# Kernel optimization log

Hardware: AMD Instinct MI355X
Metric: run time of the kernel (lower is better)

## Reference

```python
import jax, jax.numpy as jnp
import numpy as np

B, A, G = 256, 64, 978          # batch, n_atoms, num_gene
D_DRUG, D_CELL, D_DOSE = 128, 50, 128
CELL_IN, DOSE_IN = 978, 12
GLOBAL = D_DRUG + D_CELL + D_DOSE   # 306
EXP_IN = GLOBAL + 128               # 434
E, TOP_K = 4, 2


def setup_inputs() -> dict:
    key = jax.random.key(0)
    ks = jax.random.split(key, 24)
    w = lambda k, s: jax.random.normal(k, s, jnp.float32) * 0.05
    return {
        "drug_atom_embed": jax.random.normal(ks[0], (B, A, D_DRUG), jnp.float32),
        "input_cell_gex": jax.random.normal(ks[1], (B, CELL_IN), jnp.float32),
        "input_pert_idose": jax.random.normal(ks[2], (B, DOSE_IN), jnp.float32),
        # LinearEncoder: 978 -> 200 -> 100 -> 50 (ReLU after each)
        "cell_W1": w(ks[3], (CELL_IN, 200)), "cell_b1": jnp.zeros((200,), jnp.float32),
        "cell_W2": w(ks[4], (200, 100)),     "cell_b2": jnp.zeros((100,), jnp.float32),
        "cell_W3": w(ks[5], (100, D_CELL)),  "cell_b3": jnp.zeros((D_CELL,), jnp.float32),
        # DoseEncoder: 12 -> 64 -> 128 (ReLU after each; dropout off at eval)
        "dose_W1": w(ks[6], (DOSE_IN, 64)),  "dose_b1": jnp.zeros((64,), jnp.float32),
        "dose_W2": w(ks[7], (64, D_DOSE)),   "dose_b2": jnp.zeros((D_DOSE,), jnp.float32),
        # gene index embedding [num_gene, 128]
        "gene_emb": w(ks[8], (G, 128)),
        # GatingNetwork: 306 -> 128 -> 4
        "gate_W1": w(ks[9], (GLOBAL, 128)),  "gate_b1": jnp.zeros((128,), jnp.float32),
        "gate_W2": w(ks[10], (128, E)),      "gate_b2": jnp.zeros((E,), jnp.float32),
        # 4 ExpertNetworks stacked: 434 -> 128 -> 1
        "exp_W1": w(ks[11], (E, EXP_IN, 128)), "exp_b1": jnp.zeros((E, 128), jnp.float32),
        "exp_W2": w(ks[12], (E, 128, 1)),      "exp_b2": jnp.zeros((E, 1), jnp.float32),
    }


def reference(drug_atom_embed, input_cell_gex, input_pert_idose,
              cell_W1, cell_b1, cell_W2, cell_b2, cell_W3, cell_b3,
              dose_W1, dose_b1, dose_W2, dose_b2, gene_emb,
              gate_W1, gate_b1, gate_W2, gate_b2,
              exp_W1, exp_b1, exp_W2, exp_b2):
    relu = jax.nn.relu
    # drug: sum atom embeddings -> [B, 128]
    drug = drug_atom_embed.sum(axis=1)
    # cell encoder -> [B, 50]
    cell = relu(input_cell_gex @ cell_W1 + cell_b1)
    cell = relu(cell @ cell_W2 + cell_b2)
    cell = relu(cell @ cell_W3 + cell_b3)
    # dose encoder -> [B, 128]
    dose = relu(input_pert_idose @ dose_W1 + dose_b1)
    dose = relu(dose @ dose_W2 + dose_b2)
    # global features [B, 306]
    g = jnp.concatenate([drug, cell, dose], axis=1)
    # gating: top-k sparse gates [B, E]
    logits = relu(g @ gate_W1 + gate_b1) @ gate_W2 + gate_b2
    top_v, top_i = jax.lax.top_k(logits, TOP_K)
    top_g = jax.nn.softmax(top_v, axis=1)
    gates = jnp.zeros_like(logits).at[jnp.arange(logits.shape[0])[:, None], top_i].set(top_g)
    # gene-aware expert input [B, G, 434]
    expert_input = jnp.concatenate([
        jnp.broadcast_to(g[:, None, :], (g.shape[0], G, GLOBAL)),
        jnp.broadcast_to(gene_emb[None, :, :], (g.shape[0], G, 128)),
    ], axis=2)
    # all experts: [B, E, G, 128] -> [B, E, G]
    h = relu(jnp.einsum('bgi,eih->begh', expert_input, exp_W1) + exp_b1[None, :, None, :])
    o = jnp.einsum('begh,eho->beg', h, exp_W2) + exp_b2[None, :, :1]  # exp_b2[e,0] broadcast
    predictions = jnp.einsum('beg,be->bg', o, gates)
    return predictions, cell
```

## Files before the change

### kernel.cpp

```cpp
#include <hip/hip_runtime.h>

#define NB 256
#define NA 64
#define NG 978
#define CELL_IN 978
#define DOSE_IN 12
#define GLOBAL_F 306
#define EXP_IN 434
#define NE 4

#define WS_SEL 0
#define WS_U   (WS_SEL + NB*4)
#define WS_V   (WS_U + NB*256)

#define A_BLOCKS 256
#define AB_GRID  (NB + A_BLOCKS)

__device__ __forceinline__ float wave_reduce(float p) {
    #pragma unroll
    for (int off = 32; off > 0; off >>= 1) p += __shfl_down(p, off, 64);
    return p;
}

__global__ __launch_bounds__(1024) void ab_kernel(
    const float* __restrict__ drug, const float* __restrict__ gex,
    const float* __restrict__ idose,
    const float* __restrict__ cW1, const float* __restrict__ cb1,
    const float* __restrict__ cW2, const float* __restrict__ cb2,
    const float* __restrict__ cW3, const float* __restrict__ cb3,
    const float* __restrict__ dW1, const float* __restrict__ db1,
    const float* __restrict__ dW2, const float* __restrict__ db2,
    const float* __restrict__ gW1, const float* __restrict__ gb1,
    const float* __restrict__ gW2, const float* __restrict__ gb2,
    const float* __restrict__ eW1, const float* __restrict__ eb1,
    const float* __restrict__ gene,
    float* __restrict__ ws, float* __restrict__ cell_out)
{
    __shared__ float s_gex[CELL_IN];
    __shared__ float s_g[GLOBAL_F];
    __shared__ float s_h1[200];
    __shared__ float s_h2[100];
    __shared__ float s_gh[128];
    __shared__ float s_d1[64];
    __shared__ int   s_isel[2];
    __shared__ float s_part[16 * 200];
    __shared__ float s_pu[32 * 128];
    __shared__ float s_gene[64 * 129];

    const int blk = blockIdx.x, tid = threadIdx.x;

    if (blk >= NB) {
        const int ablk = blk - NB;
        const int tile = ablk >> 4, e = (ablk >> 2) & 3, hq = ablk & 3;

        for (int i = tid; i < 64 * 128; i += 1024) {
            int gl = i >> 7, k = i & 127;
            int g = tile * 64 + gl;
            s_gene[gl * 129 + k] = (g < NG) ? gene[g * 128 + k] : 0.f;
        }
        __syncthreads();

        const int slice = tid >> 6, g_in = tid & 63;
        const int h0 = hq * 32 + slice * 2;
        const float* wbase = eW1 + ((size_t)e * EXP_IN + GLOBAL_F) * 128 + h0;
        float a0 = 0.f, a1 = 0.f;
        #pragma unroll 8
        for (int k = 0; k < 128; ++k) {
            float x = s_gene[g_in * 129 + k];
            float2 w = *(const float2*)(wbase + (size_t)k * 128);
            a0 += x * w.x; a1 += x * w.y;
        }
        float* vout = ws + WS_V + ((size_t)tile * 512 + e * 128 + h0) * 64 + g_in;
        vout[0]  = a0;
        vout[64] = a1;
        return;
    }

    const int b = blk;

    if (tid < CELL_IN) s_gex[tid] = gex[b * CELL_IN + tid];
    {
        int row = tid >> 7, d = tid & 127;
        const float* p = drug + ((size_t)b * NA) * 128 + d;
        float acc = 0.f;
        #pragma unroll
        for (int i = 0; i < 8; ++i) acc += p[(size_t)(i * 8 + row) * 128];
        s_pu[row * 128 + d] = acc;
    }
    __syncthreads();
    if (tid < 128) {
        float a = 0.f;
        #pragma unroll
        for (int r = 0; r < 8; ++r) a += s_pu[r * 128 + tid];
        s_g[tid] = a;
    } else if (tid < 192) {
        int j = tid - 128;
        float acc = db1[j];
        #pragma unroll
        for (int i = 0; i < DOSE_IN; ++i)
            acc += idose[b * DOSE_IN + i] * dW1[i * 64 + j];
        s_d1[j] = fmaxf(acc, 0.f);
    }
    __syncthreads();
    if (tid < 128) {
        float acc = db2[tid];
        #pragma unroll 8
        for (int i = 0; i < 64; ++i) acc += s_d1[i] * dW2[i * 128 + tid];
        s_g[178 + tid] = fmaxf(acc, 0.f);
    }
    __syncthreads();

    {
        int q = tid & 63, ks = tid >> 6;
        if (q < 50) {
            int i0 = ks * 62, i1 = min(i0 + 62, CELL_IN);
            float4 acc = {0.f, 0.f, 0.f, 0.f};
            #pragma unroll 4
            for (int i = i0; i < i1; ++i) {
                float4 w = *(const float4*)(cW1 + (size_t)i * 200 + 4 * q);
                float x = s_gex[i];
                acc.x += x * w.x; acc.y += x * w.y; acc.z += x * w.z; acc.w += x * w.w;
            }
            *(float4*)(&s_part[ks * 200 + 4 * q]) = acc;
        }
    }
    __syncthreads();
    if (tid < 200) {
        float a = cb1[tid];
        #pragma unroll
        for (int ks = 0; ks < 16; ++ks) a += s_part[ks * 200 + tid];
        s_h1[tid] = fmaxf(a, 0.f);
    }
    __syncthreads();

    {
        int q = tid & 31, ks = tid >> 5;
        if (q < 25 && ks < 16) {
            int i0 = ks * 13, i1 = min(i0 + 13, 200);
            float4 acc = {0.f, 0.f, 0.f, 0.f};
            #pragma unroll
            for (int i = i0; i < i1; ++i) {
                float4 w = *(const float4*)(cW2 + (size_t)i * 100 + 4 * q);
                float x = s_h1[i];
                acc.x += x * w.x; acc.y += x * w.y; acc.z += x * w.z; acc.w += x * w.w;
            }
            *(float4*)(&s_part[ks * 100 + 4 * q]) = acc;
        }
    }
    __syncthreads();
    if (tid < 100) {
        float a = cb2[tid];
        #pragma unroll
        for (int ks = 0; ks < 16; ++ks) a += s_part[ks * 100 + tid];
        s_h2[tid] = fmaxf(a, 0.f);
    }
    __syncthreads();

    {
        int j = tid & 63, ks = tid >> 6;
        if (j < 50 && ks < 8) {
            int i0 = ks * 13, i1 = min(i0 + 13, 100);
            float acc = 0.f;
            #pragma unroll
            for (int i = i0; i < i1; ++i) acc += s_h2[i] * cW3[i * 50 + j];
            s_part[ks * 64 + j] = acc;
        }
    }
    __syncthreads();
    if (tid < 50) {
        float a = cb3[tid];
        #pragma unroll
        for (int ks = 0; ks < 8; ++ks) a += s_part[ks * 64 + tid];
        float r = fmaxf(a, 0.f);
        s_g[128 + tid] = r;
        cell_out[b * 50 + tid] = r;
    }
    __syncthreads();

    {
        int q = tid & 31, ks = tid >> 5;
        if (ks < 16) {
            int i0 = ks * 20, i1 = min(i0 + 20, GLOBAL_F);
            float4 acc = {0.f, 0.f, 0.f, 0.f};
            #pragma unroll
            for (int i = i0; i < i1; ++i) {
                float4 w = *(const float4*)(gW1 + (size_t)i * 128 + 4 * q);
                float x = s_g[i];
                acc.x += x * w.x; acc.y += x * w.y; acc.z += x * w.z; acc.w += x * w.w;
            }
            *(float4*)(&s_part[ks * 128 + 4 * q]) = acc;
        }
    }
    __syncthreads();
    if (tid < 128) {
        float a = gb1[tid];
        #pragma unroll
        for (int ks = 0; ks < 16; ++ks) a += s_part[ks * 128 + tid];
        s_gh[tid] = fmaxf(a, 0.f);
    }
    __syncthreads();

    if (tid < 64) {
        float h0 = s_gh[tid], h1 = s_gh[tid + 64];
        float logit[NE];
        #pragma unroll
        for (int j = 0; j < NE; ++j) {
            float p = h0 * gW2[tid * NE + j] + h1 * gW2[(tid + 64) * NE + j];
            p = wave_reduce(p);
            logit[j] = p + gb2[j];
        }
        if (tid == 0) {
            int i1 = 0; float v1 = logit[0];
            #pragma unroll
            for (int i = 1; i < NE; ++i) if (logit[i] > v1) { v1 = logit[i]; i1 = i; }
            int i2 = -1; float v2 = -__builtin_inff();
            #pragma unroll
            for (int i = 0; i < NE; ++i) {
                if (i == i1) continue;
                if (logit[i] > v2) { v2 = logit[i]; i2 = i; }
            }
            float ex = __expf(v2 - v1);
            float inv = 1.f / (1.f + ex);
            s_isel[0] = i1; s_isel[1] = i2;
            ws[WS_SEL + b * 4 + 0] = (float)i1;
            ws[WS_SEL + b * 4 + 1] = (float)i2;
            ws[WS_SEL + b * 4 + 2] = inv;
            ws[WS_SEL + b * 4 + 3] = ex * inv;
        }
    }
    __syncthreads();

    {
        int es = tid >> 9, ks = (tid >> 5) & 15, h4 = tid & 31;
        int e = s_isel[es];
        int i0 = ks * 20, i1 = min(i0 + 20, GLOBAL_F);
        const float* wp = eW1 + (size_t)e * EXP_IN * 128 + 4 * h4;
        float4 acc = {0.f, 0.f, 0.f, 0.f};
        #pragma unroll
        for (int i = i0; i < i1; ++i) {
            float4 w = *(const float4*)(wp + (size_t)i * 128);
            float x = s_g[i];
            acc.x += x * w.x; acc.y += x * w.y; acc.z += x * w.z; acc.w += x * w.w;
        }
        *(float4*)(&s_pu[(es * 16 + ks) * 128 + 4 * h4]) = acc;
    }
    __syncthreads();
    if (tid < 256) {
        int es = tid >> 7, h = tid & 127;
        int e = s_isel[es];
        float a = eb1[e * 128 + h];
        #pragma unroll
        for (int ks = 0; ks < 16; ++ks) a += s_pu[(es * 16 + ks) * 128 + h];
        ws[WS_U + (size_t)b * 256 + es * 128 + h] = a;
    }
}

__global__ __launch_bounds__(256) void c_kernel(
    const float* __restrict__ eW2, const float* __restrict__ eb2,
    const float* __restrict__ ws, float* __restrict__ pred)
{
    __shared__ float s_u[256];
    __shared__ float s_w2[256];
    const int b = blockIdx.x >> 2, quad = blockIdx.x & 3, tid = threadIdx.x;

    const int ea = (int)ws[WS_SEL + b * 4 + 0];
    const int eb = (int)ws[WS_SEL + b * 4 + 1];
    const float gA = ws[WS_SEL + b * 4 + 2];
    const float gB = ws[WS_SEL + b * 4 + 3];
    const float bA = eb2[ea], bB = eb2[eb];

    s_u[tid] = ws[WS_U + (size_t)b * 256 + tid];
    s_w2[tid] = (tid < 128) ? eW2[ea * 128 + tid] : eW2[eb * 128 + (tid - 128)];
    __syncthreads();

    const int wv = tid >> 6, lane = tid & 63;
    const int tile = quad * 4 + wv;
    const float* vA = ws + WS_V + ((size_t)tile * 512 + ea * 128) * 64 + lane;
    const float* vB = ws + WS_V + ((size_t)tile * 512 + eb * 128) * 64 + lane;

    float dA = 0.f, dB = 0.f;
    #pragma unroll 8
    for (int h = 0; h < 128; ++h) {
        dA += fmaxf(s_u[h]       + vA[(size_t)h * 64], 0.f) * s_w2[h];
        dB += fmaxf(s_u[128 + h] + vB[(size_t)h * 64], 0.f) * s_w2[128 + h];
    }
    const int g = tile * 64 + lane;
    if (g < NG) pred[(size_t)b * NG + g] = gA * (dA + bA) + gB * (dB + bB);
}

extern "C" void kernel_launch(void* const* d_in, const int* in_sizes, int n_in,
                              void* d_out, int out_size, void* d_ws, size_t ws_size,
                              hipStream_t stream) {
    const float* drug  = (const float*)d_in[0];
    const float* gex   = (const float*)d_in[1];
    const float* idose = (const float*)d_in[2];
    const float* cW1 = (const float*)d_in[3];  const float* cb1 = (const float*)d_in[4];
    const float* cW2 = (const float*)d_in[5];  const float* cb2 = (const float*)d_in[6];
    const float* cW3 = (const float*)d_in[7];  const float* cb3 = (const float*)d_in[8];
    const float* dW1 = (const float*)d_in[9];  const float* db1 = (const float*)d_in[10];
    const float* dW2 = (const float*)d_in[11]; const float* db2 = (const float*)d_in[12];
    const float* gene = (const float*)d_in[13];
    const float* gW1 = (const float*)d_in[14]; const float* gb1 = (const float*)d_in[15];
    const float* gW2 = (const float*)d_in[16]; const float* gb2 = (const float*)d_in[17];
    const float* eW1 = (const float*)d_in[18]; const float* eb1 = (const float*)d_in[19];
    const float* eW2 = (const float*)d_in[20]; const float* eb2 = (const float*)d_in[21];

    float* ws   = (float*)d_ws;
    float* out  = (float*)d_out;
    float* pred = out;
    float* cell = out + NB * NG;

    ab_kernel<<<AB_GRID, 1024, 0, stream>>>(drug, gex, idose,
        cW1, cb1, cW2, cb2, cW3, cb3, dW1, db1, dW2, db2,
        gW1, gb1, gW2, gb2, eW1, eb1, gene, ws, cell);
    c_kernel<<<NB * 4, 256, 0, stream>>>(eW2, eb2, ws, pred);
}
```

Measured before the change: 152.2 us.

## Split gene-projection kernel, process two batch rows per block, fuse expert output stage

Moves the gene-embedding projection into its own kernel. The per-sample encoder/gating kernel now handles two batch rows per block so each weight load is reused for both rows. The final expert-output computation (formerly c_kernel) is fused into the tail of the per-sample kernel, so U vectors and gate selections stay in shared memory instead of going through the workspace. The trade-off is only 128 blocks for the main kernel, so parallelism drops and the fused output stage runs serially over 16 waves per block.

```diff
diff --git a/kernel.cpp b/kernel.cpp
--- a/kernel.cpp
+++ b/kernel.cpp
@@ -13,16 +13,43 @@
 #define WS_U   (WS_SEL + NB*4)
 #define WS_V   (WS_U + NB*256)
 
-#define A_BLOCKS 256
-#define AB_GRID  (NB + A_BLOCKS)
-
 __device__ __forceinline__ float wave_reduce(float p) {
     #pragma unroll
     for (int off = 32; off > 0; off >>= 1) p += __shfl_down(p, off, 64);
     return p;
 }
 
-__global__ __launch_bounds__(1024) void ab_kernel(
+__global__ __launch_bounds__(1024) void v_kernel(
+    const float* __restrict__ gene, const float* __restrict__ eW1,
+    float* __restrict__ ws)
+{
+    __shared__ float s_gene[64 * 129];
+    const int ablk = blockIdx.x, tid = threadIdx.x;
+    const int tile = ablk >> 4, e = (ablk >> 2) & 3, hq = ablk & 3;
+
+    for (int i = tid; i < 64 * 128; i += 1024) {
+        int gl = i >> 7, k = i & 127;
+        int g = tile * 64 + gl;
+        s_gene[gl * 129 + k] = (g < NG) ? gene[g * 128 + k] : 0.f;
+    }
+    __syncthreads();
+
+    const int slice = tid >> 6, g_in = tid & 63;
+    const int h0 = hq * 32 + slice * 2;
+    const float* wbase = eW1 + ((size_t)e * EXP_IN + GLOBAL_F) * 128 + h0;
+    float a0 = 0.f, a1 = 0.f;
+    #pragma unroll 8
+    for (int k = 0; k < 128; ++k) {
+        float x = s_gene[g_in * 129 + k];
+        float2 w = *(const float2*)(wbase + (size_t)k * 128);
+        a0 += x * w.x; a1 += x * w.y;
+    }
+    float* vout = ws + WS_V + ((size_t)tile * 512 + e * 128 + h0) * 64 + g_in;
+    vout[0]  = a0;
+    vout[64] = a1;
+}
+
+__global__ __launch_bounds__(1024) void b2_kernel(
     const float* __restrict__ drug, const float* __restrict__ gex,
     const float* __restrict__ idose,
     const float* __restrict__ cW1, const float* __restrict__ cb1,
@@ -33,80 +60,63 @@
     const float* __restrict__ gW1, const float* __restrict__ gb1,
     const float* __restrict__ gW2, const float* __restrict__ gb2,
     const float* __restrict__ eW1, const float* __restrict__ eb1,
-    const float* __restrict__ gene,
-    float* __restrict__ ws, float* __restrict__ cell_out)
+    const float* __restrict__ eW2, const float* __restrict__ eb2,
+    const float* __restrict__ ws, float* __restrict__ pred,
+    float* __restrict__ cell_out)
 {
-    __shared__ float s_gex[CELL_IN];
-    __shared__ float s_g[GLOBAL_F];
-    __shared__ float s_h1[200];
-    __shared__ float s_h2[100];
-    __shared__ float s_gh[128];
-    __shared__ float s_d1[64];
-    __shared__ int   s_isel[2];
-    __shared__ float s_part[16 * 200];
-    __shared__ float s_pu[32 * 128];
-    __shared__ float s_gene[64 * 129];
+    __shared__ float s_gex[2 * CELL_IN];
+    __shared__ float s_g[2 * GLOBAL_F];
+    __shared__ float s_h1[2 * 200];
+    __shared__ float s_h2[2 * 100];
+    __shared__ float s_gh[2 * 128];
+    __shared__ float s_d1[2 * 64];
+    __shared__ int   s_isel[4];
+    __shared__ float s_gatev[4];
+    __shared__ float s_part[2 * 16 * 200];
+    __shared__ float s_pu[2 * 2 * 8 * 128];
+    __shared__ float s_u[2 * 256];
+    __shared__ float s_w2[2 * 256];
 
     const int blk = blockIdx.x, tid = threadIdx.x;
-
-    if (blk >= NB) {
-        const int ablk = blk - NB;
-        const int tile = ablk >> 4, e = (ablk >> 2) & 3, hq = ablk & 3;
-
-        for (int i = tid; i < 64 * 128; i += 1024) {
-            int gl = i >> 7, k = i & 127;
-            int g = tile * 64 + gl;
-            s_gene[gl * 129 + k] = (g < NG) ? gene[g * 128 + k] : 0.f;
-        }
-        __syncthreads();
-
-        const int slice = tid >> 6, g_in = tid & 63;
-        const int h0 = hq * 32 + slice * 2;
-        const float* wbase = eW1 + ((size_t)e * EXP_IN + GLOBAL_F) * 128 + h0;
-        float a0 = 0.f, a1 = 0.f;
-        #pragma unroll 8
-        for (int k = 0; k < 128; ++k) {
-            float x = s_gene[g_in * 129 + k];
-            float2 w = *(const float2*)(wbase + (size_t)k * 128);
-            a0 += x * w.x; a1 += x * w.y;
-        }
-        float* vout = ws + WS_V + ((size_t)tile * 512 + e * 128 + h0) * 64 + g_in;
-        vout[0]  = a0;
-        vout[64] = a1;
-        return;
-    }
-
-    const int b = blk;
-
-    if (tid < CELL_IN) s_gex[tid] = gex[b * CELL_IN + tid];
+    const int b0 = blk * 2;
+
+    for (int i = tid; i < 2 * CELL_IN; i += 1024)
+        s_gex[i] = gex[(size_t)b0 * CELL_IN + i];
     {
         int row = tid >> 7, d = tid & 127;
-        const float* p = drug + ((size_t)b * NA) * 128 + d;
-        float acc = 0.f;
-        #pragma unroll
-        for (int i = 0; i < 8; ++i) acc += p[(size_t)(i * 8 + row) * 128];
-        s_pu[row * 128 + d] = acc;
-    }
-    __syncthreads();
-    if (tid < 128) {
+        const float* p0 = drug + ((size_t)b0 * NA) * 128 + d;
+        const float* p1 = p0 + (size_t)NA * 128;
+        float a0 = 0.f, a1 = 0.f;
+        #pragma unroll
+        for (int i = 0; i < 8; ++i) {
+            a0 += p0[(size_t)(i * 8 + row) * 128];
+            a1 += p1[(size_t)(i * 8 + row) * 128];
+        }
+        s_pu[row * 128 + d] = a0;
+        s_pu[1024 + row * 128 + d] = a1;
+    }
+    __syncthreads();
+    if (tid < 256) {
+        int b = tid >> 7, d = tid & 127;
         float a = 0.f;
         #pragma unroll
-        for (int r = 0; r < 8; ++r) a += s_pu[r * 128 + tid];
-        s_g[tid] = a;
-    } else if (tid < 192) {
-        int j = tid - 128;
+        for (int r = 0; r < 8; ++r) a += s_pu[b * 1024 + r * 128 + d];
+        s_g[b * GLOBAL_F + d] = a;
+    } else if (tid < 384) {
+        int t = tid - 256, db = t >> 6, j = t & 63;
         float acc = db1[j];
         #pragma unroll
         for (int i = 0; i < DOSE_IN; ++i)
-            acc += idose[b * DOSE_IN + i] * dW1[i * 64 + j];
-        s_d1[j] = fmaxf(acc, 0.f);
-    }
-    __syncthreads();
-    if (tid < 128) {
-        float acc = db2[tid];
+            acc += idose[(b0 + db) * DOSE_IN + i] * dW1[i * 64 + j];
+        s_d1[db * 64 + j] = fmaxf(acc, 0.f);
+    }
+    __syncthreads();
+    if (tid < 256) {
+        int db = tid >> 7, j = tid & 127;
+        float acc = db2[j];
         #pragma unroll 8
-        for (int i = 0; i < 64; ++i) acc += s_d1[i] * dW2[i * 128 + tid];
-        s_g[178 + tid] = fmaxf(acc, 0.f);
+        for (int i = 0; i < 64; ++i) acc += s_d1[db * 64 + i] * dW2[i * 128 + j];
+        s_g[db * GLOBAL_F + 178 + j] = fmaxf(acc, 0.f);
     }
     __syncthreads();
 
@@ -114,102 +124,121 @@
         int q = tid & 63, ks = tid >> 6;
         if (q < 50) {
             int i0 = ks * 62, i1 = min(i0 + 62, CELL_IN);
-            float4 acc = {0.f, 0.f, 0.f, 0.f};
+            float4 a0 = {0.f,0.f,0.f,0.f}, a1 = {0.f,0.f,0.f,0.f};
             #pragma unroll 4
             for (int i = i0; i < i1; ++i) {
                 float4 w = *(const float4*)(cW1 + (size_t)i * 200 + 4 * q);
-                float x = s_gex[i];
-                acc.x += x * w.x; acc.y += x * w.y; acc.z += x * w.z; acc.w += x * w.w;
-            }
-            *(float4*)(&s_part[ks * 200 + 4 * q]) = acc;
-        }
-    }
-    __syncthreads();
-    if (tid < 200) {
-        float a = cb1[tid];
-        #pragma unroll
-        for (int ks = 0; ks < 16; ++ks) a += s_part[ks * 200 + tid];
-        s_h1[tid] = fmaxf(a, 0.f);
-    }
-    __syncthreads();
-
-    {
+                float x0 = s_gex[i], x1 = s_gex[CELL_IN + i];
+                a0.x += x0*w.x; a0.y += x0*w.y; a0.z += x0*w.z; a0.w += x0*w.w;
+                a1.x += x1*w.x; a1.y += x1*w.y; a1.z += x1*w.z; a1.w += x1*w.w;
+            }
+            *(float4*)(&s_part[ks * 200 + 4 * q]) = a0;
+            *(float4*)(&s_part[3200 + ks * 200 + 4 * q]) = a1;
+        }
+    }
+    __syncthreads();
+    if (tid < 512) {
+        int b = tid >> 8, j = tid & 255;
+        if (j < 200) {
+            float a = cb1[j];
+            #pragma unroll
+            for (int ks = 0; ks < 16; ++ks) a += s_part[b * 3200 + ks * 200 + j];
+            s_h1[b * 200 + j] = fmaxf(a, 0.f);
+        }
+    }
+    __syncthreads();
+
+    if (tid < 512) {
         int q = tid & 31, ks = tid >> 5;
-        if (q < 25 && ks < 16) {
+        if (q < 25) {
             int i0 = ks * 13, i1 = min(i0 + 13, 200);
-            float4 acc = {0.f, 0.f, 0.f, 0.f};
+            float4 a0 = {0.f,0.f,0.f,0.f}, a1 = {0.f,0.f,0.f,0.f};
             #pragma unroll
             for (int i = i0; i < i1; ++i) {
                 float4 w = *(const float4*)(cW2 + (size_t)i * 100 + 4 * q);
-                float x = s_h1[i];
-                acc.x += x * w.x; acc.y += x * w.y; acc.z += x * w.z; acc.w += x * w.w;
-            }
-            *(float4*)(&s_part[ks * 100 + 4 * q]) = acc;
-        }
-    }
-    __syncthreads();
-    if (tid < 100) {
-        float a = cb2[tid];
-        #pragma unroll
-        for (int ks = 0; ks < 16; ++ks) a += s_part[ks * 100 + tid];
-        s_h2[tid] = fmaxf(a, 0.f);
-    }
-    __syncthreads();
-
-    {
+                float x0 = s_h1[i], x1 = s_h1[200 + i];
+                a0.x += x0*w.x; a0.y += x0*w.y; a0.z += x0*w.z; a0.w += x0*w.w;
+                a1.x += x1*w.x; a1.y += x1*w.y; a1.z += x1*w.z; a1.w += x1*w.w;
+            }
+            *(float4*)(&s_part[ks * 100 + 4 * q]) = a0;
+            *(float4*)(&s_part[1600 + ks * 100 + 4 * q]) = a1;
+        }
+    }
+    __syncthreads();
+    if (tid < 256) {
+        int b = tid >> 7, j = tid & 127;
+        if (j < 100) {
+            float a = cb2[j];
+            #pragma unroll
+            for (int ks = 0; ks < 16; ++ks) a += s_part[b * 1600 + ks * 100 + j];
+            s_h2[b * 100 + j] = fmaxf(a, 0.f);
+        }
+    }
+    __syncthreads();
+
+    if (tid < 512) {
         int j = tid & 63, ks = tid >> 6;
-        if (j < 50 && ks < 8) {
+        if (j < 50) {
             int i0 = ks * 13, i1 = min(i0 + 13, 100);
-            float acc = 0.f;
-            #pragma unroll
-            for (int i = i0; i < i1; ++i) acc += s_h2[i] * cW3[i * 50 + j];
-            s_part[ks * 64 + j] = acc;
-        }
-    }
-    __syncthreads();
-    if (tid < 50) {
-        float a = cb3[tid];
-        #pragma unroll
-        for (int ks = 0; ks < 8; ++ks) a += s_part[ks * 64 + tid];
-        float r = fmaxf(a, 0.f);
-        s_g[128 + tid] = r;
-        cell_out[b * 50 + tid] = r;
-    }
-    __syncthreads();
-
-    {
+            float a0 = 0.f, a1 = 0.f;
+            #pragma unroll
+            for (int i = i0; i < i1; ++i) {
+                float w = cW3[i * 50 + j];
+                a0 += s_h2[i] * w; a1 += s_h2[100 + i] * w;
+            }
+            s_part[ks * 64 + j] = a0;
+            s_part[512 + ks * 64 + j] = a1;
+        }
+    }
+    __syncthreads();
+    if (tid < 128) {
+        int b = tid >> 6, j = tid & 63;
+        if (j < 50) {
+            float a = cb3[j];
+            #pragma unroll
+            for (int ks = 0; ks < 8; ++ks) a += s_part[b * 512 + ks * 64 + j];
+            float r = fmaxf(a, 0.f);
+            s_g[b * GLOBAL_F + 128 + j] = r;
+            cell_out[(b0 + b) * 50 + j] = r;
+        }
+    }
+    __syncthreads();
+
+    if (tid < 512) {
         int q = tid & 31, ks = tid >> 5;
-        if (ks < 16) {
-            int i0 = ks * 20, i1 = min(i0 + 20, GLOBAL_F);
-            float4 acc = {0.f, 0.f, 0.f, 0.f};
-            #pragma unroll
-            for (int i = i0; i < i1; ++i) {
-                float4 w = *(const float4*)(gW1 + (size_t)i * 128 + 4 * q);
-                float x = s_g[i];
-                acc.x += x * w.x; acc.y += x * w.y; acc.z += x * w.z; acc.w += x * w.w;
-            }
-            *(float4*)(&s_part[ks * 128 + 4 * q]) = acc;
-        }
-    }
-    __syncthreads();
+        int i0 = ks * 20, i1 = min(i0 + 20, GLOBAL_F);
+        float4 a0 = {0.f,0.f,0.f,0.f}, a1 = {0.f,0.f,0.f,0.f};
+        #pragma unroll
+        for (int i = i0; i < i1; ++i) {
+            float4 w = *(const float4*)(gW1 + (size_t)i * 128 + 4 * q);
+            float x0 = s_g[i], x1 = s_g[GLOBAL_F + i];
+            a0.x += x0*w.x; a0.y += x0*w.y; a0.z += x0*w.z; a0.w += x0*w.w;
+            a1.x += x1*w.x; a1.y += x1*w.y; a1.z += x1*w.z; a1.w += x1*w.w;
+        }
+        *(float4*)(&s_part[ks * 128 + 4 * q]) = a0;
+        *(float4*)(&s_part[2048 + ks * 128 + 4 * q]) = a1;
+    }
+    __syncthreads();
+    if (tid < 256) {
+        int b = tid >> 7, j = tid & 127;
+        float a = gb1[j];
+        #pragma unroll
+        for (int ks = 0; ks < 16; ++ks) a += s_part[b * 2048 + ks * 128 + j];
+        s_gh[b * 128 + j] = fmaxf(a, 0.f);
+    }
+    __syncthreads();
+
     if (tid < 128) {
-        float a = gb1[tid];
-        #pragma unroll
-        for (int ks = 0; ks < 16; ++ks) a += s_part[ks * 128 + tid];
-        s_gh[tid] = fmaxf(a, 0.f);
-    }
-    __syncthreads();
-
-    if (tid < 64) {
-        float h0 = s_gh[tid], h1 = s_gh[tid + 64];
+        int w = tid >> 6, lane = tid & 63;
+        float h0 = s_gh[w * 128 + lane], h1 = s_gh[w * 128 + 64 + lane];
         float logit[NE];
         #pragma unroll
         for (int j = 0; j < NE; ++j) {
-            float p = h0 * gW2[tid * NE + j] + h1 * gW2[(tid + 64) * NE + j];
+            float p = h0 * gW2[lane * NE + j] + h1 * gW2[(lane + 64) * NE + j];
             p = wave_reduce(p);
             logit[j] = p + gb2[j];
         }
-        if (tid == 0) {
+        if (lane == 0) {
             int i1 = 0; float v1 = logit[0];
             #pragma unroll
             for (int i = 1; i < NE; ++i) if (logit[i] > v1) { v1 = logit[i]; i1 = i; }
@@ -221,71 +250,65 @@
             }
             float ex = __expf(v2 - v1);
             float inv = 1.f / (1.f + ex);
-            s_isel[0] = i1; s_isel[1] = i2;
-            ws[WS_SEL + b * 4 + 0] = (float)i1;
-            ws[WS_SEL + b * 4 + 1] = (float)i2;
-            ws[WS_SEL + b * 4 + 2] = inv;
-            ws[WS_SEL + b * 4 + 3] = ex * inv;
+            s_isel[w * 2 + 0] = i1; s_isel[w * 2 + 1] = i2;
+            s_gatev[w * 2 + 0] = inv; s_gatev[w * 2 + 1] = ex * inv;
         }
     }
     __syncthreads();
 
     {
-        int es = tid >> 9, ks = (tid >> 5) & 15, h4 = tid & 31;
-        int e = s_isel[es];
-        int i0 = ks * 20, i1 = min(i0 + 20, GLOBAL_F);
+        int grp = tid >> 8;
+        int gb = grp >> 1, es = grp & 1;
+        int ks = (tid >> 5) & 7, h4 = tid & 31;
+        int e = s_isel[gb * 2 + es];
+        int i0 = ks * 39, i1 = min(i0 + 39, GLOBAL_F);
         const float* wp = eW1 + (size_t)e * EXP_IN * 128 + 4 * h4;
-        float4 acc = {0.f, 0.f, 0.f, 0.f};
-        #pragma unroll
+        const float* gp = s_g + gb * GLOBAL_F;
+        float4 acc = {0.f,0.f,0.f,0.f};
+        #pragma unroll 4
         for (int i = i0; i < i1; ++i) {
             float4 w = *(const float4*)(wp + (size_t)i * 128);
-            float x = s_g[i];
-            acc.x += x * w.x; acc.y += x * w.y; acc.z += x * w.z; acc.w += x * w.w;
-        }
-        *(float4*)(&s_pu[(es * 16 + ks) * 128 + 4 * h4]) = acc;
-    }
-    __syncthreads();
-    if (tid < 256) {
-        int es = tid >> 7, h = tid & 127;
-        int e = s_isel[es];
+            float x = gp[i];
+            acc.x += x*w.x; acc.y += x*w.y; acc.z += x*w.z; acc.w += x*w.w;
+        }
+        *(float4*)(&s_pu[(grp * 8 + ks) * 128 + 4 * h4]) = acc;
+    }
+    __syncthreads();
+    if (tid < 512) {
+        int gb = tid >> 8, es = (tid >> 7) & 1, h = tid & 127;
+        int e = s_isel[gb * 2 + es];
         float a = eb1[e * 128 + h];
-        #pragma unroll
-        for (int ks = 0; ks < 16; ++ks) a += s_pu[(es * 16 + ks) * 128 + h];
-        ws[WS_U + (size_t)b * 256 + es * 128 + h] = a;
-    }
-}
-
-__global__ __launch_bounds__(256) void c_kernel(
-    const float* __restrict__ eW2, const float* __restrict__ eb2,
-    const float* __restrict__ ws, float* __restrict__ pred)
-{
-    __shared__ float s_u[256];
-    __shared__ float s_w2[256];
-    const int b = blockIdx.x >> 2, quad = blockIdx.x & 3, tid = threadIdx.x;
-
-    const int ea = (int)ws[WS_SEL + b * 4 + 0];
-    const int eb = (int)ws[WS_SEL + b * 4 + 1];
-    const float gA = ws[WS_SEL + b * 4 + 2];
-    const float gB = ws[WS_SEL + b * 4 + 3];
-    const float bA = eb2[ea], bB = eb2[eb];
-
-    s_u[tid] = ws[WS_U + (size_t)b * 256 + tid];
-    s_w2[tid] = (tid < 128) ? eW2[ea * 128 + tid] : eW2[eb * 128 + (tid - 128)];
-    __syncthreads();
-
-    const int wv = tid >> 6, lane = tid & 63;
-    const int tile = quad * 4 + wv;
-    const float* vA = ws + WS_V + ((size_t)tile * 512 + ea * 128) * 64 + lane;
-    const float* vB = ws + WS_V + ((size_t)tile * 512 + eb * 128) * 64 + lane;
-
-    float dA = 0.f, dB = 0.f;
-    #pragma unroll 8
-    for (int h = 0; h < 128; ++h) {
-        dA += fmaxf(s_u[h]       + vA[(size_t)h * 64], 0.f) * s_w2[h];
-        dB += fmaxf(s_u[128 + h] + vB[(size_t)h * 64], 0.f) * s_w2[128 + h];
-    }
-    const int g = tile * 64 + lane;
-    if (g < NG) pred[(size_t)b * NG + g] = gA * (dA + bA) + gB * (dB + bB);
+        int grp = gb * 2 + es;
+        #pragma unroll
+        for (int ks = 0; ks < 8; ++ks) a += s_pu[(grp * 8 + ks) * 128 + h];
+        s_u[gb * 256 + es * 128 + h] = a;
+        s_w2[gb * 256 + es * 128 + h] = eW2[e * 128 + h];
+    }
+    __syncthreads();
+
+    {
+        int wv = tid >> 6, lane = tid & 63;
+        int g = wv * 64 + lane;
+        if (g < NG) {
+            #pragma unroll
+            for (int bi = 0; bi < 2; ++bi) {
+                int eA = s_isel[bi * 2 + 0], eB = s_isel[bi * 2 + 1];
+                float gA = s_gatev[bi * 2 + 0], gB = s_gatev[bi * 2 + 1];
+                float bA = eb2[eA], bB = eb2[eB];
+                const float* vA = ws + WS_V + ((size_t)wv * 512 + eA * 128) * 64 + lane;
+                const float* vB = ws + WS_V + ((size_t)wv * 512 + eB * 128) * 64 + lane;
+                const float* uu = s_u + bi * 256;
+                const float* ww = s_w2 + bi * 256;
+                float dA = 0.f, dB = 0.f;
+                #pragma unroll 8
+                for (int h = 0; h < 128; ++h) {
+                    dA += fmaxf(uu[h]       + vA[(size_t)h * 64], 0.f) * ww[h];
+                    dB += fmaxf(uu[128 + h] + vB[(size_t)h * 64], 0.f) * ww[128 + h];
+                }
+                pred[(size_t)(b0 + bi) * NG + g] = gA * (dA + bA) + gB * (dB + bB);
+            }
+        }
+    }
 }
 
 extern "C" void kernel_launch(void* const* d_in, const int* in_sizes, int n_in,
@@ -310,8 +333,8 @@
     float* pred = out;
     float* cell = out + NB * NG;
 
-    ab_kernel<<<AB_GRID, 1024, 0, stream>>>(drug, gex, idose,
+    v_kernel<<<256, 1024, 0, stream>>>(gene, eW1, ws);
+    b2_kernel<<<NB / 2, 1024, 0, stream>>>(drug, gex, idose,
         cW1, cb1, cW2, cb2, cW3, cb3, dW1, db1, dW2, db2,
-        gW1, gb1, gW2, gb2, eW1, eb1, gene, ws, cell);
-    c_kernel<<<NB * 4, 256, 0, stream>>>(eW2, eb2, ws, pred);
+        gW1, gb1, gW2, gb2, eW1, eb1, eW2, eb2, ws, pred, cell);
 }
```

New measurement: 172.4 us. 13.2% more time.

## Split cell encoder first layer into batched GEMM kernel with split-K

Applied to the files above, without the earlier changes.

Moves the 978x200 first cell-encoder layer out of the per-sample ab_kernel blocks into a separate kernel. Each block handles 16 samples, so every cW1 weight load is reused across 16 rows instead of being re-read once per sample. The layer is split four ways along K, and ab_kernel sums the partials from the workspace. This cuts weight traffic in exchange for an extra kernel launch and a workspace round trip.

```diff
diff --git a/kernel.cpp b/kernel.cpp
--- a/kernel.cpp
+++ b/kernel.cpp
@@ -12,6 +12,7 @@
 #define WS_SEL 0
 #define WS_U   (WS_SEL + NB*4)
 #define WS_V   (WS_U + NB*256)
+#define WS_P1  (WS_V + 16*512*64)
 
 #define A_BLOCKS 256
 #define AB_GRID  (NB + A_BLOCKS)
@@ -22,10 +23,40 @@
     return p;
 }
 
+__global__ __launch_bounds__(1024) void cell1_kernel(
+    const float* __restrict__ gex, const float* __restrict__ cW1,
+    float* __restrict__ ws)
+{
+    __shared__ float s_x[16][248];
+    const int blk = blockIdx.x, tid = threadIdx.x;
+    const int m = blk >> 3, n = (blk >> 2) & 1, q = blk & 3;
+    const int b0 = m * 16, j0 = n * 100, k0 = q * 245;
+    const int klen = (q == 3) ? 243 : 245;
+
+    {
+        int r = tid >> 6, lane = tid & 63;
+        for (int kk = lane; kk < klen; kk += 64)
+            s_x[r][kk] = gex[(size_t)(b0 + r) * CELL_IN + k0 + kk];
+    }
+    __syncthreads();
+
+    const int r = tid >> 6, lane = tid & 63;
+    if (lane < 25) {
+        const float* wp = cW1 + (size_t)k0 * 200 + j0 + 4 * lane;
+        float4 acc = {0.f, 0.f, 0.f, 0.f};
+        #pragma unroll 4
+        for (int i = 0; i < klen; ++i) {
+            float x = s_x[r][i];
+            float4 w = *(const float4*)(wp + (size_t)i * 200);
+            acc.x += x * w.x; acc.y += x * w.y; acc.z += x * w.z; acc.w += x * w.w;
+        }
+        *(float4*)(ws + WS_P1 + ((size_t)(q * NB + b0 + r)) * 200 + j0 + 4 * lane) = acc;
+    }
+}
+
 __global__ __launch_bounds__(1024) void ab_kernel(
-    const float* __restrict__ drug, const float* __restrict__ gex,
-    const float* __restrict__ idose,
-    const float* __restrict__ cW1, const float* __restrict__ cb1,
+    const float* __restrict__ drug, const float* __restrict__ idose,
+    const float* __restrict__ cb1,
     const float* __restrict__ cW2, const float* __restrict__ cb2,
     const float* __restrict__ cW3, const float* __restrict__ cb3,
     const float* __restrict__ dW1, const float* __restrict__ db1,
@@ -36,7 +67,6 @@
     const float* __restrict__ gene,
     float* __restrict__ ws, float* __restrict__ cell_out)
 {
-    __shared__ float s_gex[CELL_IN];
     __shared__ float s_g[GLOBAL_F];
     __shared__ float s_h1[200];
     __shared__ float s_h2[100];
@@ -78,7 +108,6 @@
 
     const int b = blk;
 
-    if (tid < CELL_IN) s_gex[tid] = gex[b * CELL_IN + tid];
     {
         int row = tid >> 7, d = tid & 127;
         const float* p = drug + ((size_t)b * NA) * 128 + d;
@@ -108,28 +137,15 @@
         for (int i = 0; i < 64; ++i) acc += s_d1[i] * dW2[i * 128 + tid];
         s_g[178 + tid] = fmaxf(acc, 0.f);
     }
-    __syncthreads();
-
-    {
-        int q = tid & 63, ks = tid >> 6;
-        if (q < 50) {
-            int i0 = ks * 62, i1 = min(i0 + 62, CELL_IN);
-            float4 acc = {0.f, 0.f, 0.f, 0.f};
-            #pragma unroll 4
-            for (int i = i0; i < i1; ++i) {
-                float4 w = *(const float4*)(cW1 + (size_t)i * 200 + 4 * q);
-                float x = s_gex[i];
-                acc.x += x * w.x; acc.y += x * w.y; acc.z += x * w.z; acc.w += x * w.w;
-            }
-            *(float4*)(&s_part[ks * 200 + 4 * q]) = acc;
-        }
-    }
-    __syncthreads();
-    if (tid < 200) {
-        float a = cb1[tid];
-        #pragma unroll
-        for (int ks = 0; ks < 16; ++ks) a += s_part[ks * 200 + tid];
-        s_h1[tid] = fmaxf(a, 0.f);
+
+    if (tid >= 256 && tid < 456) {
+        int j = tid - 256;
+        float a = cb1[j]
+                + ws[WS_P1 + ((size_t)(0 * NB + b)) * 200 + j]
+                + ws[WS_P1 + ((size_t)(1 * NB + b)) * 200 + j]
+                + ws[WS_P1 + ((size_t)(2 * NB + b)) * 200 + j]
+                + ws[WS_P1 + ((size_t)(3 * NB + b)) * 200 + j];
+        s_h1[j] = fmaxf(a, 0.f);
     }
     __syncthreads();
 
@@ -310,8 +326,9 @@
     float* pred = out;
     float* cell = out + NB * NG;
 
-    ab_kernel<<<AB_GRID, 1024, 0, stream>>>(drug, gex, idose,
-        cW1, cb1, cW2, cb2, cW3, cb3, dW1, db1, dW2, db2,
+    cell1_kernel<<<128, 1024, 0, stream>>>(gex, cW1, ws);
+    ab_kernel<<<AB_GRID, 1024, 0, stream>>>(drug, idose, cb1,
+        cW2, cb2, cW3, cb3, dW1, db1, dW2, db2,
         gW1, gb1, gW2, gb2, eW1, eb1, gene, ws, cell);
     c_kernel<<<NB * 4, 256, 0, stream>>>(eW2, eb2, ws, pred);
 }
```

After: 170.3 us. 11.8% more time.
